# Performance work log

Measured on AMD Instinct MI355X. Metric: run time of the kernel, lower is better.

Reference implementation:

```python
import jax, jax.numpy as jnp
import numpy as np

B, S, D, H = 2, 2048, 1024, 16
HD = D // H


def setup_inputs() -> dict:
    key = jax.random.key(0)
    ks = jax.random.split(key, 9)
    std = 0.02
    return {
        "x": jax.random.normal(ks[0], (B, S, D), dtype=jnp.float32),
        "wq": jax.random.normal(ks[1], (D, D), dtype=jnp.float32) * std,
        "bq": jnp.zeros((D,), dtype=jnp.float32),
        "wk": jax.random.normal(ks[2], (D, D), dtype=jnp.float32) * std,
        "bk": jnp.zeros((D,), dtype=jnp.float32),
        "wv": jax.random.normal(ks[3], (D, D), dtype=jnp.float32) * std,
        "bv": jnp.zeros((D,), dtype=jnp.float32),
        "wo": jax.random.normal(ks[4], (D, D), dtype=jnp.float32) * std,
        "bo": jnp.zeros((D,), dtype=jnp.float32),
    }


def reference(x, wq, bq, wk, bk, wv, bv, wo, bo):
    bsz, seq_len, d_model = x.shape
    # projections: torch Linear computes x @ W.T + b with W of shape (out, in)
    q = (x @ wq.T + bq).reshape(bsz, seq_len, H, HD).transpose(0, 2, 1, 3)  # bhsd
    k = (x @ wk.T + bk).reshape(bsz, seq_len, H, HD).transpose(0, 2, 1, 3)
    v = (x @ wv.T + bv).reshape(bsz, seq_len, H, HD).transpose(0, 2, 1, 3)
    scale = HD ** -0.5
    scores = jnp.einsum("bhqd,bhkd->bhqk", q, k) * scale  # [B,H,S,S]
    causal = jnp.tril(jnp.ones((seq_len, seq_len), dtype=bool))
    scores = jnp.where(causal[None, None], scores, -jnp.inf)
    attn = jax.nn.softmax(scores, axis=-1)
    ctx = jnp.einsum("bhqk,bhkd->bhqd", attn, v)
    ctx = ctx.transpose(0, 2, 1, 3).reshape(bsz, seq_len, d_model)
    return ctx @ wo.T + bo
```

## Files before the change

### kernel.cpp

```cpp
#include <hip/hip_runtime.h>
#include <hip/hip_bf16.h>

#define B_  2
#define S_  2048
#define D_  1024
#define H_  16
#define HD_ 64
#define M_  (B_ * S_)

typedef __bf16 bf16;
typedef __bf16 bf16x4 __attribute__((ext_vector_type(4)));
typedef __bf16 bf16x8 __attribute__((ext_vector_type(8)));
typedef float  f32x4  __attribute__((ext_vector_type(4)));

__device__ __forceinline__ bf16x8 ld8g(const bf16* p) { return *(const bf16x8*)p; }

#define GLL(g, l) __builtin_amdgcn_global_load_lds( \
    (const __attribute__((address_space(1))) void*)(g), \
    (__attribute__((address_space(3))) void*)(l), 16, 0, 0)

__global__ __launch_bounds__(256) void convert_kernel(
    const float* __restrict__ x,  const float* __restrict__ wq,
    const float* __restrict__ wk, const float* __restrict__ wv,
    const float* __restrict__ wo,
    bf16* __restrict__ xb,  bf16* __restrict__ wqb, bf16* __restrict__ wkb,
    bf16* __restrict__ wvb, bf16* __restrict__ wob)
{
    const int seg = blockIdx.y;
    const float* src;
    bf16* dst;
    if (seg < 4)      { src = x  + (long)seg * 1048576; dst = xb  + (long)seg * 1048576; }
    else if (seg == 4){ src = wq; dst = wqb; }
    else if (seg == 5){ src = wk; dst = wkb; }
    else if (seg == 6){ src = wv; dst = wvb; }
    else              { src = wo; dst = wob; }
    const long i = ((long)blockIdx.x * 256 + threadIdx.x) * 8;
    float4 a = *(const float4*)(src + i);
    float4 b = *(const float4*)(src + i + 4);
    bf16x8 r;
    r[0] = (bf16)a.x; r[1] = (bf16)a.y; r[2] = (bf16)a.z; r[3] = (bf16)a.w;
    r[4] = (bf16)b.x; r[5] = (bf16)b.y; r[6] = (bf16)b.z; r[7] = (bf16)b.w;
    *(bf16x8*)(dst + i) = r;
}

__device__ __forceinline__ void gemm_acc_bk32(
    const bf16* __restrict__ A, const bf16* __restrict__ Bt,
    f32x4 (&acc)[4][4])
{
    __shared__ bf16 As[128 * 32];
    __shared__ bf16 Bs[128 * 32];

    const int tid  = threadIdx.x;
    const int wave = tid >> 6;
    const int lane = tid & 63;
    const int quad = lane >> 4;
    const int l15  = lane & 15;
    const int wr   = (wave >> 1) * 64;
    const int wc   = (wave & 1) * 64;
    const int m0   = blockIdx.y * 128;
    const int n0   = blockIdx.x * 128;

    const int sr = wave * 16 + (lane >> 2);
    const int sc = (lane & 3) * 8;
    const bf16* Ag = A  + (long)(m0 + sr) * D_ + sc;
    const bf16* Bg = Bt + (long)(n0 + sr) * D_ + sc;
    bf16* lA = As + wave * 512;
    bf16* lB = Bs + wave * 512;

    for (int k0 = 0; k0 < D_; k0 += 32) {
        __syncthreads();
        GLL(Ag + k0,             lA);
        GLL(Ag + 64 * D_ + k0,   lA + 64 * 32);
        GLL(Bg + k0,             lB);
        GLL(Bg + 64 * D_ + k0,   lB + 64 * 32);
        __syncthreads();

        bf16x8 af[4], bfr[4];
        for (int mi = 0; mi < 4; mi++)
            af[mi] = *(const bf16x8*)&As[(wr + mi * 16 + l15) * 32 + quad * 8];
        for (int ni = 0; ni < 4; ni++)
            bfr[ni] = *(const bf16x8*)&Bs[(wc + ni * 16 + l15) * 32 + quad * 8];

        for (int mi = 0; mi < 4; mi++)
            for (int ni = 0; ni < 4; ni++)
                acc[mi][ni] = __builtin_amdgcn_mfma_f32_16x16x32_bf16(
                    af[mi], bfr[ni], acc[mi][ni], 0, 0, 0);
    }
}

__global__ __launch_bounds__(256) void gemm_qkv(
    const bf16* __restrict__ xb,
    const bf16* __restrict__ wqb, const bf16* __restrict__ wkb, const bf16* __restrict__ wvb,
    const float* __restrict__ bq, const float* __restrict__ bk, const float* __restrict__ bv,
    bf16* __restrict__ qb, bf16* __restrict__ kb, bf16* __restrict__ vt)
{
    const bf16*  Bt   = (blockIdx.z == 0) ? wqb : (blockIdx.z == 1) ? wkb : wvb;
    const float* bias = (blockIdx.z == 0) ? bq  : (blockIdx.z == 1) ? bk  : bv;

    f32x4 acc[4][4] = {};
    gemm_acc_bk32(xb, Bt, acc);

    const int lane = threadIdx.x & 63;
    const int wave = threadIdx.x >> 6;
    const int quad = lane >> 4;
    const int l15  = lane & 15;
    const int wr   = (wave >> 1) * 64;
    const int wc   = (wave & 1) * 64;
    const int m0   = blockIdx.y * 128;
    const int n0   = blockIdx.x * 128;

    if (blockIdx.z < 2) {
        bf16* Cout = (blockIdx.z == 0) ? qb : kb;
        for (int ni = 0; ni < 4; ni++) {
            const int col = n0 + wc + ni * 16 + l15;
            const float bv = bias[col];
            for (int mi = 0; mi < 4; mi++) {
                const int rowb = m0 + wr + mi * 16 + quad * 4;
                for (int r = 0; r < 4; r++)
                    Cout[(long)(rowb + r) * D_ + col] = (bf16)(acc[mi][ni][r] + bv);
            }
        }
    } else {
        for (int ni = 0; ni < 4; ni++) {
            const int col = n0 + wc + ni * 16 + l15;
            const float bv = bias[col];
            const int h = col >> 6, hd = col & (HD_ - 1);
            for (int mi = 0; mi < 4; mi++) {
                const int rowb = m0 + wr + mi * 16 + quad * 4;
                const int b = rowb >> 11;
                const int s0 = rowb & (S_ - 1);
                bf16x4 v4;
                for (int r = 0; r < 4; r++) v4[r] = (bf16)(acc[mi][ni][r] + bv);
                *(bf16x4*)&vt[(((long)(b * H_ + h)) * HD_ + hd) * S_ + s0] = v4;
            }
        }
    }
}

__global__ __launch_bounds__(256) void gemm_out(
    const bf16* __restrict__ cb, const bf16* __restrict__ wob,
    const float* __restrict__ bo, float* __restrict__ out)
{
    __shared__ bf16 As[64 * 32];
    __shared__ bf16 Bs[128 * 32];

    const int tid  = threadIdx.x;
    const int wave = tid >> 6;
    const int lane = tid & 63;
    const int quad = lane >> 4;
    const int l15  = lane & 15;
    const int wr   = (wave >> 1) * 32;
    const int wc   = (wave & 1) * 64;
    const int m0   = blockIdx.y * 64;
    const int n0   = blockIdx.x * 128;

    const int sr = tid >> 2;
    const int scg = (tid & 3) * 8;
    const bf16* Ag = cb  + (long)(m0 + sr) * D_ + scg;
    const bf16* Bg = wob + (long)(n0 + sr) * D_ + scg;
    bf16* lA = As + wave * 512;
    bf16* lB = Bs + wave * 512;

    f32x4 acc[2][4] = {};
    for (int k0 = 0; k0 < D_; k0 += 32) {
        __syncthreads();
        GLL(Ag + k0,            lA);
        GLL(Bg + k0,            lB);
        GLL(Bg + 64 * D_ + k0,  lB + 64 * 32);
        __syncthreads();

        bf16x8 af[2], bfr[4];
        for (int mi = 0; mi < 2; mi++)
            af[mi] = *(const bf16x8*)&As[(wr + mi * 16 + l15) * 32 + quad * 8];
        for (int ni = 0; ni < 4; ni++)
            bfr[ni] = *(const bf16x8*)&Bs[(wc + ni * 16 + l15) * 32 + quad * 8];

        for (int mi = 0; mi < 2; mi++)
            for (int ni = 0; ni < 4; ni++)
                acc[mi][ni] = __builtin_amdgcn_mfma_f32_16x16x32_bf16(
                    af[mi], bfr[ni], acc[mi][ni], 0, 0, 0);
    }

    for (int ni = 0; ni < 4; ni++) {
        const int col = n0 + wc + ni * 16 + l15;
        const float bv = bo[col];
        for (int mi = 0; mi < 2; mi++) {
            const int rowb = m0 + wr + mi * 16 + quad * 4;
            for (int r = 0; r < 4; r++)
                out[(long)(rowb + r) * D_ + col] = acc[mi][ni][r] + bv;
        }
    }
}

__global__ __launch_bounds__(256) void attn_kernel(
    const bf16* __restrict__ Q, const bf16* __restrict__ K,
    const bf16* __restrict__ vt, bf16* __restrict__ ctx)
{
    constexpr int LDK = 72;
    __shared__ bf16 Ks[2][64 * LDK];
    __shared__ bf16 Vt[2][64 * LDK];
    __shared__ bf16 Pq[4][32 * LDK];

    const int tid  = threadIdx.x;
    const int wave = tid >> 6;
    const int lane = tid & 63;
    const int quad = lane >> 4;
    const int l15  = lane & 15;
    const int bh   = blockIdx.y;
    const int qt   = (blockIdx.y < 16) ? blockIdx.x : (15 - (int)blockIdx.x);
    const int b    = bh >> 4, h = bh & 15;
    const long base  = ((long)b * S_) * D_ + h * HD_;
    const bf16* Vth  = vt + (long)bh * HD_ * S_;

    const int r0 = tid >> 3;
    const int c0 = (tid & 7) * 8;

    const int qw    = qt * 128 + wave * 32;
    const int qrow0 = qw + l15;
    const int qrow1 = qw + 16 + l15;
    const bf16* Qr0 = Q + base + (long)qrow0 * D_;
    const bf16* Qr1 = Q + base + (long)qrow1 * D_;
    bf16x8 qf00 = ld8g(&Qr0[quad * 8]);
    bf16x8 qf01 = ld8g(&Qr0[quad * 8 + 32]);
    bf16x8 qf10 = ld8g(&Qr1[quad * 8]);
    bf16x8 qf11 = ld8g(&Qr1[quad * 8 + 32]);

    float l0 = 0.f, l1 = 0.f;
    f32x4 o0[4] = {}, o1[4] = {};

    auto process_tile = [&](int kbase, int buf) {
        if (kbase > qw + 31) return;
        f32x4 s0[4], s1[4];
        __builtin_amdgcn_s_setprio(1);
        #pragma unroll
        for (int kt = 0; kt < 4; kt++) {
            const bf16* Kr = &Ks[buf][(kt * 16 + l15) * LDK + quad * 8];
            bf16x8 a0 = *(const bf16x8*)Kr;
            bf16x8 a1 = *(const bf16x8*)(Kr + 32);
            f32x4 z0 = {}, z1 = {};
            z0 = __builtin_amdgcn_mfma_f32_16x16x32_bf16(a0, qf00, z0, 0, 0, 0);
            z0 = __builtin_amdgcn_mfma_f32_16x16x32_bf16(a1, qf01, z0, 0, 0, 0);
            z1 = __builtin_amdgcn_mfma_f32_16x16x32_bf16(a0, qf10, z1, 0, 0, 0);
            z1 = __builtin_amdgcn_mfma_f32_16x16x32_bf16(a1, qf11, z1, 0, 0, 0);
            s0[kt] = z0; s1[kt] = z1;
        }
        __builtin_amdgcn_s_setprio(0);

        float sum0 = 0.f, sum1 = 0.f;
        if (kbase + 63 > qw) {
            #pragma unroll
            for (int kt = 0; kt < 4; kt++)
                #pragma unroll
                for (int r = 0; r < 4; r++) {
                    const int k_g = kbase + kt * 16 + quad * 4 + r;
                    const float p = (k_g <= qrow0) ? __expf(s0[kt][r] * 0.125f) : 0.f;
                    s0[kt][r] = p;
                    sum0 += p;
                }
        } else {
            #pragma unroll
            for (int kt = 0; kt < 4; kt++)
                #pragma unroll
                for (int r = 0; r < 4; r++) {
                    const float p = __expf(s0[kt][r] * 0.125f);
                    s0[kt][r] = p;
                    sum0 += p;
                }
        }
        if (kbase + 63 > qw + 16) {
            #pragma unroll
            for (int kt = 0; kt < 4; kt++)
                #pragma unroll
                for (int r = 0; r < 4; r++) {
                    const int k_g = kbase + kt * 16 + quad * 4 + r;
                    const float p = (k_g <= qrow1) ? __expf(s1[kt][r] * 0.125f) : 0.f;
                    s1[kt][r] = p;
                    sum1 += p;
                }
        } else {
            #pragma unroll
            for (int kt = 0; kt < 4; kt++)
                #pragma unroll
                for (int r = 0; r < 4; r++) {
                    const float p = __expf(s1[kt][r] * 0.125f);
                    s1[kt][r] = p;
                    sum1 += p;
                }
        }
        sum0 += __shfl_xor(sum0, 16, 64);
        sum0 += __shfl_xor(sum0, 32, 64);
        l0 += sum0;
        sum1 += __shfl_xor(sum1, 16, 64);
        sum1 += __shfl_xor(sum1, 32, 64);
        l1 += sum1;

        bf16* Pw = &Pq[wave][0];
        #pragma unroll
        for (int kt = 0; kt < 4; kt++) {
            union { uint2 u; bf16 hh[4]; } p0, p1;
            p0.hh[0] = (bf16)s0[kt][0]; p0.hh[1] = (bf16)s0[kt][1];
            p0.hh[2] = (bf16)s0[kt][2]; p0.hh[3] = (bf16)s0[kt][3];
            p1.hh[0] = (bf16)s1[kt][0]; p1.hh[1] = (bf16)s1[kt][1];
            p1.hh[2] = (bf16)s1[kt][2]; p1.hh[3] = (bf16)s1[kt][3];
            *(uint2*)&Pw[l15 * LDK + kt * 16 + quad * 4] = p0.u;
            *(uint2*)&Pw[(16 + l15) * LDK + kt * 16 + quad * 4] = p1.u;
        }
        __asm__ volatile("s_waitcnt lgkmcnt(0)" ::: "memory");
        bf16x8 pf00 = *(const bf16x8*)&Pw[l15 * LDK + quad * 8];
        bf16x8 pf01 = *(const bf16x8*)&Pw[l15 * LDK + quad * 8 + 32];
        bf16x8 pf10 = *(const bf16x8*)&Pw[(16 + l15) * LDK + quad * 8];
        bf16x8 pf11 = *(const bf16x8*)&Pw[(16 + l15) * LDK + quad * 8 + 32];

        __builtin_amdgcn_s_setprio(1);
        #pragma unroll
        for (int ni = 0; ni < 4; ni++) {
            const bf16* Vr = &Vt[buf][(ni * 16 + l15) * LDK + quad * 8];
            bf16x8 av0 = *(const bf16x8*)Vr;
            bf16x8 av1 = *(const bf16x8*)(Vr + 32);
            o0[ni] = __builtin_amdgcn_mfma_f32_16x16x32_bf16(av0, pf00, o0[ni], 0, 0, 0);
            o0[ni] = __builtin_amdgcn_mfma_f32_16x16x32_bf16(av1, pf01, o0[ni], 0, 0, 0);
            o1[ni] = __builtin_amdgcn_mfma_f32_16x16x32_bf16(av0, pf10, o1[ni], 0, 0, 0);
            o1[ni] = __builtin_amdgcn_mfma_f32_16x16x32_bf16(av1, pf11, o1[ni], 0, 0, 0);
        }
        __builtin_amdgcn_s_setprio(0);
    };

    bf16x8 kA0 = ld8g(K + base + (long)r0 * D_ + c0);
    bf16x8 kA1 = ld8g(K + base + (long)(r0 + 32) * D_ + c0);
    bf16x8 wA0 = ld8g(Vth + (long)r0 * S_ + c0);
    bf16x8 wA1 = ld8g(Vth + (long)(r0 + 32) * S_ + c0);
    bf16x8 kB0 = ld8g(K + base + (long)(64 + r0) * D_ + c0);
    bf16x8 kB1 = ld8g(K + base + (long)(64 + r0 + 32) * D_ + c0);
    bf16x8 wB0 = ld8g(Vth + (long)r0 * S_ + 64 + c0);
    bf16x8 wB1 = ld8g(Vth + (long)(r0 + 32) * S_ + 64 + c0);

    const int njt = 2 * qt + 2;
    for (int j = 0; j < njt; j += 2) {
        __syncthreads();
        *(bf16x8*)&Ks[0][r0 * LDK + c0]        = kA0;
        *(bf16x8*)&Ks[0][(r0 + 32) * LDK + c0] = kA1;
        *(bf16x8*)&Vt[0][r0 * LDK + c0]        = wA0;
        *(bf16x8*)&Vt[0][(r0 + 32) * LDK + c0] = wA1;
        *(bf16x8*)&Ks[1][r0 * LDK + c0]        = kB0;
        *(bf16x8*)&Ks[1][(r0 + 32) * LDK + c0] = kB1;
        *(bf16x8*)&Vt[1][r0 * LDK + c0]        = wB0;
        *(bf16x8*)&Vt[1][(r0 + 32) * LDK + c0] = wB1;
        if (j + 2 < njt) {
            kA0 = ld8g(K + base + (long)((j + 2) * 64 + r0) * D_ + c0);
            kA1 = ld8g(K + base + (long)((j + 2) * 64 + r0 + 32) * D_ + c0);
            wA0 = ld8g(Vth + (long)r0 * S_ + (j + 2) * 64 + c0);
            wA1 = ld8g(Vth + (long)(r0 + 32) * S_ + (j + 2) * 64 + c0);
            kB0 = ld8g(K + base + (long)((j + 3) * 64 + r0) * D_ + c0);
            kB1 = ld8g(K + base + (long)((j + 3) * 64 + r0 + 32) * D_ + c0);
            wB0 = ld8g(Vth + (long)r0 * S_ + (j + 3) * 64 + c0);
            wB1 = ld8g(Vth + (long)(r0 + 32) * S_ + (j + 3) * 64 + c0);
        }
        __syncthreads();
        process_tile(j * 64, 0);
        process_tile(j * 64 + 64, 1);
    }

    const float inv0 = 1.f / l0;
    const float inv1 = 1.f / l1;
    bf16* Pw = &Pq[wave][0];
    #pragma unroll
    for (int ni = 0; ni < 4; ni++)
        #pragma unroll
        for (int r = 0; r < 4; r++) {
            Pw[l15 * LDK + ni * 16 + quad * 4 + r]        = (bf16)(o0[ni][r] * inv0);
            Pw[(16 + l15) * LDK + ni * 16 + quad * 4 + r] = (bf16)(o1[ni][r] * inv1);
        }
    __asm__ volatile("s_waitcnt lgkmcnt(0)" ::: "memory");
    #pragma unroll
    for (int round = 0; round < 4; round++) {
        const int rowq = (lane >> 3) + round * 8;
        bf16x8 val = *(const bf16x8*)&Pw[rowq * LDK + (lane & 7) * 8];
        const int q_g = qt * 128 + wave * 32 + rowq;
        *(bf16x8*)&ctx[base + (long)q_g * D_ + (lane & 7) * 8] = val;
    }
}

extern "C" void kernel_launch(void* const* d_in, const int* in_sizes, int n_in,
                              void* d_out, int out_size, void* d_ws, size_t ws_size,
                              hipStream_t stream)
{
    const float* x  = (const float*)d_in[0];
    const float* wq = (const float*)d_in[1];
    const float* bq = (const float*)d_in[2];
    const float* wk = (const float*)d_in[3];
    const float* bk = (const float*)d_in[4];
    const float* wv = (const float*)d_in[5];
    const float* bv = (const float*)d_in[6];
    const float* wo = (const float*)d_in[7];
    const float* bo = (const float*)d_in[8];
    float* out = (float*)d_out;

    const long NX = (long)M_ * D_;
    const long NW = (long)D_ * D_;
    bf16* xb  = (bf16*)d_ws;
    bf16* wqb = xb  + NX;
    bf16* wkb = wqb + NW;
    bf16* wvb = wkb + NW;
    bf16* wob = wvb + NW;
    bf16* qb  = wob + NW;
    bf16* kb  = qb  + NX;
    bf16* vt  = kb  + NX;
    bf16* cb  = xb;

    dim3 blk(256, 1, 1);

    convert_kernel<<<dim3(512, 8), blk, 0, stream>>>(
        x, wq, wk, wv, wo, xb, wqb, wkb, wvb, wob);

    gemm_qkv<<<dim3(8, 32, 3), blk, 0, stream>>>(
        xb, wqb, wkb, wvb, bq, bk, bv, qb, kb, vt);

    attn_kernel<<<dim3(16, 32), blk, 0, stream>>>(qb, kb, vt, cb);

    gemm_out<<<dim3(8, 64), blk, 0, stream>>>(cb, wob, bo, out);
}
```

Before: 185.4 us.

## Split long causal attention tiles across two blocks and add XOR-swizzled LDS layout

Each of the upper eight query tiles per head is now split into two key-range chunks handled by separate blocks. The blocks write unnormalized partial outputs and row sums to a workspace, and a new combine kernel merges them. This balances the causal workload across a larger grid. Shared-memory tiles also drop the padded stride in favour of an XOR swizzle to avoid bank conflicts. The cost is an extra kernel launch plus a float32 round trip for the partials.

```diff
diff --git a/kernel.cpp b/kernel.cpp
--- a/kernel.cpp
+++ b/kernel.cpp
@@ -18,6 +18,8 @@
 #define GLL(g, l) __builtin_amdgcn_global_load_lds( \
     (const __attribute__((address_space(1))) void*)(g), \
     (__attribute__((address_space(3))) void*)(l), 16, 0, 0)
+
+#define SWZ(row, byteoff) (((row) * 128) + ((byteoff) ^ (((row) & 7) << 4)))
 
 __global__ __launch_bounds__(256) void convert_kernel(
     const float* __restrict__ x,  const float* __restrict__ wq,
@@ -194,12 +196,12 @@
 
 __global__ __launch_bounds__(256) void attn_kernel(
     const bf16* __restrict__ Q, const bf16* __restrict__ K,
-    const bf16* __restrict__ vt, bf16* __restrict__ ctx)
-{
-    constexpr int LDK = 72;
-    __shared__ bf16 Ks[2][64 * LDK];
-    __shared__ bf16 Vt[2][64 * LDK];
-    __shared__ bf16 Pq[4][32 * LDK];
+    const bf16* __restrict__ vt, bf16* __restrict__ ctx,
+    float* __restrict__ pO, float* __restrict__ pL)
+{
+    __shared__ bf16 Ks[2][64 * 64];
+    __shared__ bf16 Vt[2][64 * 64];
+    __shared__ bf16 Pq[4][32 * 64];
 
     const int tid  = threadIdx.x;
     const int wave = tid >> 6;
@@ -207,13 +209,33 @@
     const int quad = lane >> 4;
     const int l15  = lane & 15;
     const int bh   = blockIdx.y;
-    const int qt   = (blockIdx.y < 16) ? blockIdx.x : (15 - (int)blockIdx.x);
+
+    const int xm = (bh & 1) ? (23 - (int)blockIdx.x) : (int)blockIdx.x;
+    int qt, t0, t1, slot;
+    if (xm < 8) {
+        qt = xm; t0 = 0; t1 = 2 * qt + 2; slot = -1;
+    } else {
+        const int i  = xm - 8;
+        qt = 8 + (i >> 1);
+        const int ch = i & 1;
+        const int h2 = (qt + 2) & ~1;
+        t0 = ch ? h2 : 0;
+        t1 = ch ? (2 * qt + 2) : h2;
+        slot = (((bh << 3) | (qt - 8)) << 1) | ch;
+    }
+
     const int b    = bh >> 4, h = bh & 15;
     const long base  = ((long)b * S_) * D_ + h * HD_;
+    const bf16* Kg   = K + base;
     const bf16* Vth  = vt + (long)bh * HD_ * S_;
+
+    char* K0 = (char*)&Ks[0][0]; char* K1 = (char*)&Ks[1][0];
+    char* V0 = (char*)&Vt[0][0]; char* V1 = (char*)&Vt[1][0];
+    char* Pwb = (char*)&Pq[wave][0];
 
     const int r0 = tid >> 3;
     const int c0 = (tid & 7) * 8;
+    const int cB = (tid & 7) * 16;
 
     const int qw    = qt * 128 + wave * 32;
     const int qrow0 = qw + l15;
@@ -230,13 +252,14 @@
 
     auto process_tile = [&](int kbase, int buf) {
         if (kbase > qw + 31) return;
+        const char* Kb = buf ? K1 : K0;
+        const char* Vb = buf ? V1 : V0;
         f32x4 s0[4], s1[4];
         __builtin_amdgcn_s_setprio(1);
         #pragma unroll
         for (int kt = 0; kt < 4; kt++) {
-            const bf16* Kr = &Ks[buf][(kt * 16 + l15) * LDK + quad * 8];
-            bf16x8 a0 = *(const bf16x8*)Kr;
-            bf16x8 a1 = *(const bf16x8*)(Kr + 32);
+            bf16x8 a0 = *(const bf16x8*)(Kb + SWZ(kt * 16 + l15, quad * 16));
+            bf16x8 a1 = *(const bf16x8*)(Kb + SWZ(kt * 16 + l15, quad * 16 + 64));
             f32x4 z0 = {}, z1 = {};
             z0 = __builtin_amdgcn_mfma_f32_16x16x32_bf16(a0, qf00, z0, 0, 0, 0);
             z0 = __builtin_amdgcn_mfma_f32_16x16x32_bf16(a1, qf01, z0, 0, 0, 0);
@@ -294,7 +317,6 @@
         sum1 += __shfl_xor(sum1, 32, 64);
         l1 += sum1;
 
-        bf16* Pw = &Pq[wave][0];
         #pragma unroll
         for (int kt = 0; kt < 4; kt++) {
             union { uint2 u; bf16 hh[4]; } p0, p1;
@@ -302,21 +324,20 @@
             p0.hh[2] = (bf16)s0[kt][2]; p0.hh[3] = (bf16)s0[kt][3];
             p1.hh[0] = (bf16)s1[kt][0]; p1.hh[1] = (bf16)s1[kt][1];
             p1.hh[2] = (bf16)s1[kt][2]; p1.hh[3] = (bf16)s1[kt][3];
-            *(uint2*)&Pw[l15 * LDK + kt * 16 + quad * 4] = p0.u;
-            *(uint2*)&Pw[(16 + l15) * LDK + kt * 16 + quad * 4] = p1.u;
+            *(uint2*)(Pwb + SWZ(l15,      kt * 32 + quad * 8)) = p0.u;
+            *(uint2*)(Pwb + SWZ(16 + l15, kt * 32 + quad * 8)) = p1.u;
         }
         __asm__ volatile("s_waitcnt lgkmcnt(0)" ::: "memory");
-        bf16x8 pf00 = *(const bf16x8*)&Pw[l15 * LDK + quad * 8];
-        bf16x8 pf01 = *(const bf16x8*)&Pw[l15 * LDK + quad * 8 + 32];
-        bf16x8 pf10 = *(const bf16x8*)&Pw[(16 + l15) * LDK + quad * 8];
-        bf16x8 pf11 = *(const bf16x8*)&Pw[(16 + l15) * LDK + quad * 8 + 32];
+        bf16x8 pf00 = *(const bf16x8*)(Pwb + SWZ(l15,      quad * 16));
+        bf16x8 pf01 = *(const bf16x8*)(Pwb + SWZ(l15,      quad * 16 + 64));
+        bf16x8 pf10 = *(const bf16x8*)(Pwb + SWZ(16 + l15, quad * 16));
+        bf16x8 pf11 = *(const bf16x8*)(Pwb + SWZ(16 + l15, quad * 16 + 64));
 
         __builtin_amdgcn_s_setprio(1);
         #pragma unroll
         for (int ni = 0; ni < 4; ni++) {
-            const bf16* Vr = &Vt[buf][(ni * 16 + l15) * LDK + quad * 8];
-            bf16x8 av0 = *(const bf16x8*)Vr;
-            bf16x8 av1 = *(const bf16x8*)(Vr + 32);
+            bf16x8 av0 = *(const bf16x8*)(Vb + SWZ(ni * 16 + l15, quad * 16));
+            bf16x8 av1 = *(const bf16x8*)(Vb + SWZ(ni * 16 + l15, quad * 16 + 64));
             o0[ni] = __builtin_amdgcn_mfma_f32_16x16x32_bf16(av0, pf00, o0[ni], 0, 0, 0);
             o0[ni] = __builtin_amdgcn_mfma_f32_16x16x32_bf16(av1, pf01, o0[ni], 0, 0, 0);
             o1[ni] = __builtin_amdgcn_mfma_f32_16x16x32_bf16(av0, pf10, o1[ni], 0, 0, 0);
@@ -325,33 +346,32 @@
         __builtin_amdgcn_s_setprio(0);
     };
 
-    bf16x8 kA0 = ld8g(K + base + (long)r0 * D_ + c0);
-    bf16x8 kA1 = ld8g(K + base + (long)(r0 + 32) * D_ + c0);
-    bf16x8 wA0 = ld8g(Vth + (long)r0 * S_ + c0);
-    bf16x8 wA1 = ld8g(Vth + (long)(r0 + 32) * S_ + c0);
-    bf16x8 kB0 = ld8g(K + base + (long)(64 + r0) * D_ + c0);
-    bf16x8 kB1 = ld8g(K + base + (long)(64 + r0 + 32) * D_ + c0);
-    bf16x8 wB0 = ld8g(Vth + (long)r0 * S_ + 64 + c0);
-    bf16x8 wB1 = ld8g(Vth + (long)(r0 + 32) * S_ + 64 + c0);
-
-    const int njt = 2 * qt + 2;
-    for (int j = 0; j < njt; j += 2) {
-        __syncthreads();
-        *(bf16x8*)&Ks[0][r0 * LDK + c0]        = kA0;
-        *(bf16x8*)&Ks[0][(r0 + 32) * LDK + c0] = kA1;
-        *(bf16x8*)&Vt[0][r0 * LDK + c0]        = wA0;
-        *(bf16x8*)&Vt[0][(r0 + 32) * LDK + c0] = wA1;
-        *(bf16x8*)&Ks[1][r0 * LDK + c0]        = kB0;
-        *(bf16x8*)&Ks[1][(r0 + 32) * LDK + c0] = kB1;
-        *(bf16x8*)&Vt[1][r0 * LDK + c0]        = wB0;
-        *(bf16x8*)&Vt[1][(r0 + 32) * LDK + c0] = wB1;
-        if (j + 2 < njt) {
-            kA0 = ld8g(K + base + (long)((j + 2) * 64 + r0) * D_ + c0);
-            kA1 = ld8g(K + base + (long)((j + 2) * 64 + r0 + 32) * D_ + c0);
+    bf16x8 kA0 = ld8g(Kg + (long)(t0 * 64 + r0) * D_ + c0);
+    bf16x8 kA1 = ld8g(Kg + (long)(t0 * 64 + r0 + 32) * D_ + c0);
+    bf16x8 wA0 = ld8g(Vth + (long)r0 * S_ + t0 * 64 + c0);
+    bf16x8 wA1 = ld8g(Vth + (long)(r0 + 32) * S_ + t0 * 64 + c0);
+    bf16x8 kB0 = ld8g(Kg + (long)((t0 + 1) * 64 + r0) * D_ + c0);
+    bf16x8 kB1 = ld8g(Kg + (long)((t0 + 1) * 64 + r0 + 32) * D_ + c0);
+    bf16x8 wB0 = ld8g(Vth + (long)r0 * S_ + (t0 + 1) * 64 + c0);
+    bf16x8 wB1 = ld8g(Vth + (long)(r0 + 32) * S_ + (t0 + 1) * 64 + c0);
+
+    for (int j = t0; j < t1; j += 2) {
+        __syncthreads();
+        *(bf16x8*)(K0 + SWZ(r0,      cB)) = kA0;
+        *(bf16x8*)(K0 + SWZ(r0 + 32, cB)) = kA1;
+        *(bf16x8*)(V0 + SWZ(r0,      cB)) = wA0;
+        *(bf16x8*)(V0 + SWZ(r0 + 32, cB)) = wA1;
+        *(bf16x8*)(K1 + SWZ(r0,      cB)) = kB0;
+        *(bf16x8*)(K1 + SWZ(r0 + 32, cB)) = kB1;
+        *(bf16x8*)(V1 + SWZ(r0,      cB)) = wB0;
+        *(bf16x8*)(V1 + SWZ(r0 + 32, cB)) = wB1;
+        if (j + 2 < t1) {
+            kA0 = ld8g(Kg + (long)((j + 2) * 64 + r0) * D_ + c0);
+            kA1 = ld8g(Kg + (long)((j + 2) * 64 + r0 + 32) * D_ + c0);
             wA0 = ld8g(Vth + (long)r0 * S_ + (j + 2) * 64 + c0);
             wA1 = ld8g(Vth + (long)(r0 + 32) * S_ + (j + 2) * 64 + c0);
-            kB0 = ld8g(K + base + (long)((j + 3) * 64 + r0) * D_ + c0);
-            kB1 = ld8g(K + base + (long)((j + 3) * 64 + r0 + 32) * D_ + c0);
+            kB0 = ld8g(Kg + (long)((j + 3) * 64 + r0) * D_ + c0);
+            kB1 = ld8g(Kg + (long)((j + 3) * 64 + r0 + 32) * D_ + c0);
             wB0 = ld8g(Vth + (long)r0 * S_ + (j + 3) * 64 + c0);
             wB1 = ld8g(Vth + (long)(r0 + 32) * S_ + (j + 3) * 64 + c0);
         }
@@ -360,23 +380,74 @@
         process_tile(j * 64 + 64, 1);
     }
 
+    if (slot >= 0) {
+        float* Op = pO + (long)slot * (128 * 64);
+        const int ql0 = wave * 32 + l15;
+        #pragma unroll
+        for (int ni = 0; ni < 4; ni++) {
+            *(f32x4*)&Op[(long)ql0 * 64 + ni * 16 + quad * 4]        = o0[ni];
+            *(f32x4*)&Op[(long)(ql0 + 16) * 64 + ni * 16 + quad * 4] = o1[ni];
+        }
+        if (quad == 0) {
+            pL[slot * 128 + ql0]      = l0;
+            pL[slot * 128 + ql0 + 16] = l1;
+        }
+        return;
+    }
+
     const float inv0 = 1.f / l0;
     const float inv1 = 1.f / l1;
-    bf16* Pw = &Pq[wave][0];
     #pragma unroll
     for (int ni = 0; ni < 4; ni++)
         #pragma unroll
         for (int r = 0; r < 4; r++) {
-            Pw[l15 * LDK + ni * 16 + quad * 4 + r]        = (bf16)(o0[ni][r] * inv0);
-            Pw[(16 + l15) * LDK + ni * 16 + quad * 4 + r] = (bf16)(o1[ni][r] * inv1);
+            *(bf16*)(Pwb + SWZ(l15,      ni * 32 + quad * 8 + r * 2)) = (bf16)(o0[ni][r] * inv0);
+            *(bf16*)(Pwb + SWZ(16 + l15, ni * 32 + quad * 8 + r * 2)) = (bf16)(o1[ni][r] * inv1);
         }
     __asm__ volatile("s_waitcnt lgkmcnt(0)" ::: "memory");
     #pragma unroll
     for (int round = 0; round < 4; round++) {
         const int rowq = (lane >> 3) + round * 8;
-        bf16x8 val = *(const bf16x8*)&Pw[rowq * LDK + (lane & 7) * 8];
+        bf16x8 val = *(const bf16x8*)(Pwb + SWZ(rowq, (lane & 7) * 16));
         const int q_g = qt * 128 + wave * 32 + rowq;
         *(bf16x8*)&ctx[base + (long)q_g * D_ + (lane & 7) * 8] = val;
+    }
+}
+
+__global__ __launch_bounds__(256) void combine_kernel(
+    const float* __restrict__ pO, const float* __restrict__ pL,
+    bf16* __restrict__ ctx)
+{
+    const int item = blockIdx.x;
+    const int bh = item >> 3, qt = 8 + (item & 7);
+    const int b = bh >> 4, h = bh & 15;
+    const int t = threadIdx.x;
+    const int q = t >> 1;
+    const int hd0 = (t & 1) * 32;
+    const long s0 = (long)(item * 2) * (128 * 64);
+    const long s1 = (long)(item * 2 + 1) * (128 * 64);
+    const float l = pL[(item * 2) * 128 + q] + pL[(item * 2 + 1) * 128 + q];
+    const float inv = 1.f / l;
+    const float* O0 = pO + s0 + (long)q * 64 + hd0;
+    const float* O1 = pO + s1 + (long)q * 64 + hd0;
+    const int q_g = qt * 128 + q;
+    bf16* dst = ctx + ((long)b * S_) * D_ + h * HD_ + (long)q_g * D_ + hd0;
+    #pragma unroll
+    for (int i = 0; i < 4; i++) {
+        f32x4 a  = ((const f32x4*)O0)[2 * i];
+        f32x4 a2 = ((const f32x4*)O0)[2 * i + 1];
+        f32x4 c  = ((const f32x4*)O1)[2 * i];
+        f32x4 c2 = ((const f32x4*)O1)[2 * i + 1];
+        bf16x8 r;
+        r[0] = (bf16)((a[0]  + c[0])  * inv);
+        r[1] = (bf16)((a[1]  + c[1])  * inv);
+        r[2] = (bf16)((a[2]  + c[2])  * inv);
+        r[3] = (bf16)((a[3]  + c[3])  * inv);
+        r[4] = (bf16)((a2[0] + c2[0]) * inv);
+        r[5] = (bf16)((a2[1] + c2[1]) * inv);
+        r[6] = (bf16)((a2[2] + c2[2]) * inv);
+        r[7] = (bf16)((a2[3] + c2[3]) * inv);
+        *(bf16x8*)(dst + i * 8) = r;
     }
 }
 
@@ -406,6 +477,8 @@
     bf16* kb  = qb  + NX;
     bf16* vt  = kb  + NX;
     bf16* cb  = xb;
+    float* pO = (float*)(vt + NX);
+    float* pL = pO + (long)512 * 128 * 64;
 
     dim3 blk(256, 1, 1);
 
@@ -415,7 +488,9 @@
     gemm_qkv<<<dim3(8, 32, 3), blk, 0, stream>>>(
         xb, wqb, wkb, wvb, bq, bk, bv, qb, kb, vt);
 
-    attn_kernel<<<dim3(16, 32), blk, 0, stream>>>(qb, kb, vt, cb);
+    attn_kernel<<<dim3(24, 32), blk, 0, stream>>>(qb, kb, vt, cb, pO, pL);
+
+    combine_kernel<<<dim3(256, 1, 1), blk, 0, stream>>>(pO, pL, cb);
 
     gemm_out<<<dim3(8, 64), blk, 0, stream>>>(cb, wob, bo, out);
 }
```

New measurement: 200.7 us. +8.3%, slower.

## Switch attention to 32x32x16 MFMA with register-resident P and swizzled LDS

Applied to the files above, without the earlier changes.

Rewrites the attention inner loop to use 32x32x16 bf16 MFMA instructions, so each wave handles 32 query rows as a single tile. The softmax probabilities are repacked in registers with a cross-half lane shuffle instead of a round trip through per-wave LDS scratch. K/V shared tiles drop the padded stride for an XOR-swizzled 128-byte row layout to avoid bank conflicts, and the epilogue reuses the K buffer. This cuts LDS traffic and frees shared memory, at the cost of more shuffles and more complex index math that must match the MFMA output layout exactly.

```diff
diff --git a/kernel.cpp b/kernel.cpp
--- a/kernel.cpp
+++ b/kernel.cpp
@@ -12,12 +12,16 @@
 typedef __bf16 bf16x4 __attribute__((ext_vector_type(4)));
 typedef __bf16 bf16x8 __attribute__((ext_vector_type(8)));
 typedef float  f32x4  __attribute__((ext_vector_type(4)));
+typedef float  f32x16 __attribute__((ext_vector_type(16)));
+typedef unsigned int uint;
 
 __device__ __forceinline__ bf16x8 ld8g(const bf16* p) { return *(const bf16x8*)p; }
 
 #define GLL(g, l) __builtin_amdgcn_global_load_lds( \
     (const __attribute__((address_space(1))) void*)(g), \
     (__attribute__((address_space(3))) void*)(l), 16, 0, 0)
+
+#define SWZ(row, byteoff) (((row) * 128) + ((byteoff) ^ (((row) & 7) << 4)))
 
 __global__ __launch_bounds__(256) void convert_kernel(
     const float* __restrict__ x,  const float* __restrict__ wq,
@@ -196,162 +200,135 @@
     const bf16* __restrict__ Q, const bf16* __restrict__ K,
     const bf16* __restrict__ vt, bf16* __restrict__ ctx)
 {
-    constexpr int LDK = 72;
-    __shared__ bf16 Ks[2][64 * LDK];
-    __shared__ bf16 Vt[2][64 * LDK];
-    __shared__ bf16 Pq[4][32 * LDK];
+    __shared__ bf16 Ks[2][64 * 64];
+    __shared__ bf16 Vt[2][64 * 64];
 
     const int tid  = threadIdx.x;
     const int wave = tid >> 6;
     const int lane = tid & 63;
-    const int quad = lane >> 4;
-    const int l15  = lane & 15;
+    const int l31  = lane & 31;
+    const int hi   = lane >> 5;
+    const int hi16 = hi * 16;
+    const int hi4  = hi * 4;
     const int bh   = blockIdx.y;
     const int qt   = (blockIdx.y < 16) ? blockIdx.x : (15 - (int)blockIdx.x);
     const int b    = bh >> 4, h = bh & 15;
-    const long base  = ((long)b * S_) * D_ + h * HD_;
-    const bf16* Vth  = vt + (long)bh * HD_ * S_;
+    const long base = ((long)b * S_) * D_ + h * HD_;
+    const bf16* Kg  = K + base;
+    const bf16* Vth = vt + (long)bh * HD_ * S_;
+
+    char* K0 = (char*)&Ks[0][0]; char* K1 = (char*)&Ks[1][0];
+    char* V0 = (char*)&Vt[0][0]; char* V1 = (char*)&Vt[1][0];
 
     const int r0 = tid >> 3;
     const int c0 = (tid & 7) * 8;
-
-    const int qw    = qt * 128 + wave * 32;
-    const int qrow0 = qw + l15;
-    const int qrow1 = qw + 16 + l15;
-    const bf16* Qr0 = Q + base + (long)qrow0 * D_;
-    const bf16* Qr1 = Q + base + (long)qrow1 * D_;
-    bf16x8 qf00 = ld8g(&Qr0[quad * 8]);
-    bf16x8 qf01 = ld8g(&Qr0[quad * 8 + 32]);
-    bf16x8 qf10 = ld8g(&Qr1[quad * 8]);
-    bf16x8 qf11 = ld8g(&Qr1[quad * 8 + 32]);
-
-    float l0 = 0.f, l1 = 0.f;
-    f32x4 o0[4] = {}, o1[4] = {};
+    const int cB = (tid & 7) * 16;
+
+    const int qw   = qt * 128 + wave * 32;
+    const int qrow = qw + l31;
+    const bf16* Qr = Q + base + (long)qrow * D_;
+    bf16x8 qf0 = ld8g(Qr + 0  + hi * 8);
+    bf16x8 qf1 = ld8g(Qr + 16 + hi * 8);
+    bf16x8 qf2 = ld8g(Qr + 32 + hi * 8);
+    bf16x8 qf3 = ld8g(Qr + 48 + hi * 8);
+
+    float l_i = 0.f;
+    f32x16 oA = {}, oB = {};
 
     auto process_tile = [&](int kbase, int buf) {
         if (kbase > qw + 31) return;
-        f32x4 s0[4], s1[4];
-        __builtin_amdgcn_s_setprio(1);
+        const char* Kb = buf ? K1 : K0;
+        const char* Vb = buf ? V1 : V0;
         #pragma unroll
-        for (int kt = 0; kt < 4; kt++) {
-            const bf16* Kr = &Ks[buf][(kt * 16 + l15) * LDK + quad * 8];
-            bf16x8 a0 = *(const bf16x8*)Kr;
-            bf16x8 a1 = *(const bf16x8*)(Kr + 32);
-            f32x4 z0 = {}, z1 = {};
-            z0 = __builtin_amdgcn_mfma_f32_16x16x32_bf16(a0, qf00, z0, 0, 0, 0);
-            z0 = __builtin_amdgcn_mfma_f32_16x16x32_bf16(a1, qf01, z0, 0, 0, 0);
-            z1 = __builtin_amdgcn_mfma_f32_16x16x32_bf16(a0, qf10, z1, 0, 0, 0);
-            z1 = __builtin_amdgcn_mfma_f32_16x16x32_bf16(a1, qf11, z1, 0, 0, 0);
-            s0[kt] = z0; s1[kt] = z1;
-        }
-        __builtin_amdgcn_s_setprio(0);
-
-        float sum0 = 0.f, sum1 = 0.f;
-        if (kbase + 63 > qw) {
+        for (int s = 0; s < 2; s++) {
+            const int kb = kbase + 32 * s;
+            if (kb > qw + 31) continue;
+            f32x16 sa = {};
+            __builtin_amdgcn_s_setprio(1);
+            {
+                bf16x8 a0 = *(const bf16x8*)(Kb + SWZ(32 * s + l31, 0   + hi16));
+                bf16x8 a1 = *(const bf16x8*)(Kb + SWZ(32 * s + l31, 32  + hi16));
+                bf16x8 a2 = *(const bf16x8*)(Kb + SWZ(32 * s + l31, 64  + hi16));
+                bf16x8 a3 = *(const bf16x8*)(Kb + SWZ(32 * s + l31, 96  + hi16));
+                sa = __builtin_amdgcn_mfma_f32_32x32x16_bf16(a0, qf0, sa, 0, 0, 0);
+                sa = __builtin_amdgcn_mfma_f32_32x32x16_bf16(a1, qf1, sa, 0, 0, 0);
+                sa = __builtin_amdgcn_mfma_f32_32x32x16_bf16(a2, qf2, sa, 0, 0, 0);
+                sa = __builtin_amdgcn_mfma_f32_32x32x16_bf16(a3, qf3, sa, 0, 0, 0);
+            }
+            __builtin_amdgcn_s_setprio(0);
+
+            float p[16];
+            float loc = 0.f;
+            if (kb + 31 <= qw) {
+                #pragma unroll
+                for (int r = 0; r < 16; r++) { p[r] = __expf(sa[r] * 0.125f); loc += p[r]; }
+            } else {
+                #pragma unroll
+                for (int r = 0; r < 16; r++) {
+                    const int kg = kb + (r & 3) + 8 * (r >> 2) + hi4;
+                    p[r] = (kg <= qrow) ? __expf(sa[r] * 0.125f) : 0.f;
+                    loc += p[r];
+                }
+            }
+            l_i += loc + __shfl_xor(loc, 32, 64);
+
+            uint w[8], sw[8];
             #pragma unroll
-            for (int kt = 0; kt < 4; kt++)
-                #pragma unroll
-                for (int r = 0; r < 4; r++) {
-                    const int k_g = kbase + kt * 16 + quad * 4 + r;
-                    const float p = (k_g <= qrow0) ? __expf(s0[kt][r] * 0.125f) : 0.f;
-                    s0[kt][r] = p;
-                    sum0 += p;
-                }
-        } else {
+            for (int t = 0; t < 8; t++) {
+                union { uint u; bf16 h2[2]; } pk;
+                pk.h2[0] = (bf16)p[2 * t];
+                pk.h2[1] = (bf16)p[2 * t + 1];
+                w[t] = pk.u;
+            }
             #pragma unroll
-            for (int kt = 0; kt < 4; kt++)
-                #pragma unroll
-                for (int r = 0; r < 4; r++) {
-                    const float p = __expf(s0[kt][r] * 0.125f);
-                    s0[kt][r] = p;
-                    sum0 += p;
-                }
-        }
-        if (kbase + 63 > qw + 16) {
+            for (int t = 0; t < 8; t++)
+                sw[t] = (uint)__shfl_xor((int)w[t], 32, 64);
+
+            __builtin_amdgcn_s_setprio(1);
             #pragma unroll
-            for (int kt = 0; kt < 4; kt++)
-                #pragma unroll
-                for (int r = 0; r < 4; r++) {
-                    const int k_g = kbase + kt * 16 + quad * 4 + r;
-                    const float p = (k_g <= qrow1) ? __expf(s1[kt][r] * 0.125f) : 0.f;
-                    s1[kt][r] = p;
-                    sum1 += p;
-                }
-        } else {
-            #pragma unroll
-            for (int kt = 0; kt < 4; kt++)
-                #pragma unroll
-                for (int r = 0; r < 4; r++) {
-                    const float p = __expf(s1[kt][r] * 0.125f);
-                    s1[kt][r] = p;
-                    sum1 += p;
-                }
-        }
-        sum0 += __shfl_xor(sum0, 16, 64);
-        sum0 += __shfl_xor(sum0, 32, 64);
-        l0 += sum0;
-        sum1 += __shfl_xor(sum1, 16, 64);
-        sum1 += __shfl_xor(sum1, 32, 64);
-        l1 += sum1;
-
-        bf16* Pw = &Pq[wave][0];
-        #pragma unroll
-        for (int kt = 0; kt < 4; kt++) {
-            union { uint2 u; bf16 hh[4]; } p0, p1;
-            p0.hh[0] = (bf16)s0[kt][0]; p0.hh[1] = (bf16)s0[kt][1];
-            p0.hh[2] = (bf16)s0[kt][2]; p0.hh[3] = (bf16)s0[kt][3];
-            p1.hh[0] = (bf16)s1[kt][0]; p1.hh[1] = (bf16)s1[kt][1];
-            p1.hh[2] = (bf16)s1[kt][2]; p1.hh[3] = (bf16)s1[kt][3];
-            *(uint2*)&Pw[l15 * LDK + kt * 16 + quad * 4] = p0.u;
-            *(uint2*)&Pw[(16 + l15) * LDK + kt * 16 + quad * 4] = p1.u;
-        }
-        __asm__ volatile("s_waitcnt lgkmcnt(0)" ::: "memory");
-        bf16x8 pf00 = *(const bf16x8*)&Pw[l15 * LDK + quad * 8];
-        bf16x8 pf01 = *(const bf16x8*)&Pw[l15 * LDK + quad * 8 + 32];
-        bf16x8 pf10 = *(const bf16x8*)&Pw[(16 + l15) * LDK + quad * 8];
-        bf16x8 pf11 = *(const bf16x8*)&Pw[(16 + l15) * LDK + quad * 8 + 32];
-
-        __builtin_amdgcn_s_setprio(1);
-        #pragma unroll
-        for (int ni = 0; ni < 4; ni++) {
-            const bf16* Vr = &Vt[buf][(ni * 16 + l15) * LDK + quad * 8];
-            bf16x8 av0 = *(const bf16x8*)Vr;
-            bf16x8 av1 = *(const bf16x8*)(Vr + 32);
-            o0[ni] = __builtin_amdgcn_mfma_f32_16x16x32_bf16(av0, pf00, o0[ni], 0, 0, 0);
-            o0[ni] = __builtin_amdgcn_mfma_f32_16x16x32_bf16(av1, pf01, o0[ni], 0, 0, 0);
-            o1[ni] = __builtin_amdgcn_mfma_f32_16x16x32_bf16(av0, pf10, o1[ni], 0, 0, 0);
-            o1[ni] = __builtin_amdgcn_mfma_f32_16x16x32_bf16(av1, pf11, o1[ni], 0, 0, 0);
-        }
-        __builtin_amdgcn_s_setprio(0);
+            for (int cc = 0; cc < 2; cc++) {
+                union { uint u[4]; bf16x8 v; } pa;
+                pa.u[0] = hi ? sw[4 * cc + 2] : w[4 * cc];
+                pa.u[1] = hi ? sw[4 * cc + 3] : w[4 * cc + 1];
+                pa.u[2] = hi ? w[4 * cc + 2]  : sw[4 * cc];
+                pa.u[3] = hi ? w[4 * cc + 3]  : sw[4 * cc + 1];
+                const int kc = 2 * s + cc;
+                bf16x8 vb0 = *(const bf16x8*)(Vb + SWZ(l31,      kc * 32 + hi16));
+                bf16x8 vb1 = *(const bf16x8*)(Vb + SWZ(32 + l31, kc * 32 + hi16));
+                oA = __builtin_amdgcn_mfma_f32_32x32x16_bf16(pa.v, vb0, oA, 0, 0, 0);
+                oB = __builtin_amdgcn_mfma_f32_32x32x16_bf16(pa.v, vb1, oB, 0, 0, 0);
+            }
+            __builtin_amdgcn_s_setprio(0);
+        }
     };
 
-    bf16x8 kA0 = ld8g(K + base + (long)r0 * D_ + c0);
-    bf16x8 kA1 = ld8g(K + base + (long)(r0 + 32) * D_ + c0);
+    bf16x8 kA0 = ld8g(Kg + (long)r0 * D_ + c0);
+    bf16x8 kA1 = ld8g(Kg + (long)(r0 + 32) * D_ + c0);
     bf16x8 wA0 = ld8g(Vth + (long)r0 * S_ + c0);
     bf16x8 wA1 = ld8g(Vth + (long)(r0 + 32) * S_ + c0);
-    bf16x8 kB0 = ld8g(K + base + (long)(64 + r0) * D_ + c0);
-    bf16x8 kB1 = ld8g(K + base + (long)(64 + r0 + 32) * D_ + c0);
+    bf16x8 kB0 = ld8g(Kg + (long)(64 + r0) * D_ + c0);
+    bf16x8 kB1 = ld8g(Kg + (long)(64 + r0 + 32) * D_ + c0);
     bf16x8 wB0 = ld8g(Vth + (long)r0 * S_ + 64 + c0);
     bf16x8 wB1 = ld8g(Vth + (long)(r0 + 32) * S_ + 64 + c0);
 
     const int njt = 2 * qt + 2;
     for (int j = 0; j < njt; j += 2) {
         __syncthreads();
-        *(bf16x8*)&Ks[0][r0 * LDK + c0]        = kA0;
-        *(bf16x8*)&Ks[0][(r0 + 32) * LDK + c0] = kA1;
-        *(bf16x8*)&Vt[0][r0 * LDK + c0]        = wA0;
-        *(bf16x8*)&Vt[0][(r0 + 32) * LDK + c0] = wA1;
-        *(bf16x8*)&Ks[1][r0 * LDK + c0]        = kB0;
-        *(bf16x8*)&Ks[1][(r0 + 32) * LDK + c0] = kB1;
-        *(bf16x8*)&Vt[1][r0 * LDK + c0]        = wB0;
-        *(bf16x8*)&Vt[1][(r0 + 32) * LDK + c0] = wB1;
+        *(bf16x8*)(K0 + SWZ(r0,      cB)) = kA0;
+        *(bf16x8*)(K0 + SWZ(r0 + 32, cB)) = kA1;
+        *(bf16x8*)(V0 + SWZ(r0,      cB)) = wA0;
+        *(bf16x8*)(V0 + SWZ(r0 + 32, cB)) = wA1;
+        *(bf16x8*)(K1 + SWZ(r0,      cB)) = kB0;
+        *(bf16x8*)(K1 + SWZ(r0 + 32, cB)) = kB1;
+        *(bf16x8*)(V1 + SWZ(r0,      cB)) = wB0;
+        *(bf16x8*)(V1 + SWZ(r0 + 32, cB)) = wB1;
         if (j + 2 < njt) {
-            kA0 = ld8g(K + base + (long)((j + 2) * 64 + r0) * D_ + c0);
-            kA1 = ld8g(K + base + (long)((j + 2) * 64 + r0 + 32) * D_ + c0);
+            kA0 = ld8g(Kg + (long)((j + 2) * 64 + r0) * D_ + c0);
+            kA1 = ld8g(Kg + (long)((j + 2) * 64 + r0 + 32) * D_ + c0);
             wA0 = ld8g(Vth + (long)r0 * S_ + (j + 2) * 64 + c0);
             wA1 = ld8g(Vth + (long)(r0 + 32) * S_ + (j + 2) * 64 + c0);
-            kB0 = ld8g(K + base + (long)((j + 3) * 64 + r0) * D_ + c0);
-            kB1 = ld8g(K + base + (long)((j + 3) * 64 + r0 + 32) * D_ + c0);
+            kB0 = ld8g(Kg + (long)((j + 3) * 64 + r0) * D_ + c0);
+            kB1 = ld8g(Kg + (long)((j + 3) * 64 + r0 + 32) * D_ + c0);
             wB0 = ld8g(Vth + (long)r0 * S_ + (j + 3) * 64 + c0);
             wB1 = ld8g(Vth + (long)(r0 + 32) * S_ + (j + 3) * 64 + c0);
         }
@@ -360,21 +337,21 @@
         process_tile(j * 64 + 64, 1);
     }
 
-    const float inv0 = 1.f / l0;
-    const float inv1 = 1.f / l1;
-    bf16* Pw = &Pq[wave][0];
+    __syncthreads();
+    char* epi = (char*)&Ks[0][0] + wave * 4096;
+    const float inv = 1.f / l_i;
     #pragma unroll
-    for (int ni = 0; ni < 4; ni++)
-        #pragma unroll
-        for (int r = 0; r < 4; r++) {
-            Pw[l15 * LDK + ni * 16 + quad * 4 + r]        = (bf16)(o0[ni][r] * inv0);
-            Pw[(16 + l15) * LDK + ni * 16 + quad * 4 + r] = (bf16)(o1[ni][r] * inv1);
-        }
+    for (int r = 0; r < 16; r++) {
+        const int qr = (r & 3) + 8 * (r >> 2) + hi4;
+        const float si = __shfl(inv, qr, 64);
+        *(bf16*)(epi + SWZ(qr, l31 * 2))      = (bf16)(oA[r] * si);
+        *(bf16*)(epi + SWZ(qr, 64 + l31 * 2)) = (bf16)(oB[r] * si);
+    }
     __asm__ volatile("s_waitcnt lgkmcnt(0)" ::: "memory");
     #pragma unroll
     for (int round = 0; round < 4; round++) {
         const int rowq = (lane >> 3) + round * 8;
-        bf16x8 val = *(const bf16x8*)&Pw[rowq * LDK + (lane & 7) * 8];
+        bf16x8 val = *(const bf16x8*)(epi + SWZ(rowq, (lane & 7) * 16));
         const int q_g = qt * 128 + wave * 32 + rowq;
         *(bf16x8*)&ctx[base + (long)q_g * D_ + (lane & 7) * 8] = val;
     }
```

After: 191.2 us. 3.1% more time.
